# Optimization experiments

Hardware: AMD Instinct MI355X
Metric: run time of the kernel (lower is better)

Reference implementation:

```python
import jax, jax.numpy as jnp
import numpy as np

FP8_MAX = 448.0  # float8_e4m3fn max representable value


def _fp8_quant(v):
    """Snap values to the fp8 e4m3 grid (saturating), return fp32."""
    v = jnp.clip(v, -FP8_MAX, FP8_MAX)
    return v.astype(jnp.float8_e4m3fn).astype(jnp.float32)


def setup_inputs() -> dict:
    key = jax.random.key(0)
    k1, k2, k3 = jax.random.split(key, 3)
    N_TOK, D_IN, D_OUT = 8192, 4096, 4096
    x = jax.random.normal(k1, (N_TOK, D_IN), dtype=jnp.float32)
    # weight is stored already quantized to fp8 in the real module; snap to grid
    w = jax.random.normal(k2, (D_OUT, D_IN), dtype=jnp.float32)
    weight_scale = jnp.array([2.0 / FP8_MAX], dtype=jnp.float32)  # per-tensor
    weight = _fp8_quant(w / weight_scale)  # fp8-grid values, kept in fp32
    bias = jax.random.normal(k3, (D_OUT,), dtype=jnp.float32)
    input_scale = jnp.array([4.0 / FP8_MAX], dtype=jnp.float32)  # per-tensor act scale
    return {"x": x, "weight": weight, "weight_scale": weight_scale,
            "bias": bias, "input_scale": input_scale}


def reference(x, weight, weight_scale, bias, input_scale):
    # quantize_activation_per_tensor_fp8: x/scale -> clamp -> fp8 e4m3
    qinput = _fp8_quant(x / input_scale)  # [N, D_in], fp8-grid values
    acc = jnp.einsum('nk,ok->no', qinput, weight)  # fp32 accumulate
    out = acc * (input_scale * weight_scale) + bias
    return out.astype(x.dtype)
```

## Files before the change

kernel.cpp:

```cpp
#include <hip/hip_runtime.h>
#include <stdint.h>

#define FP8_MAX 448.0f

typedef float floatx16 __attribute__((ext_vector_type(16)));
typedef int   intx4    __attribute__((ext_vector_type(4)));
typedef int   intx8    __attribute__((ext_vector_type(8)));

__device__ __forceinline__ void async_copy16(const void* g, void* s) {
    __builtin_amdgcn_global_load_lds(
        (const __attribute__((address_space(1))) void*)g,
        (__attribute__((address_space(3))) void*)s,
        16, 0, 0);
}

__global__ void __launch_bounds__(256) quant_fp8_kernel(
    const float* __restrict__ x, const float* __restrict__ w,
    const float* __restrict__ scale,
    uint8_t* __restrict__ qx, uint8_t* __restrict__ qw,
    long nx4, long ntot4)
{
    const float invx = 1.0f / scale[0];
    const long stride = (long)gridDim.x * 256;
    for (long g = (long)blockIdx.x * 256 + threadIdx.x; g < ntot4; g += stride) {
        const float4* src; int* dst; float inv; long idx;
        if (g < nx4) { src = (const float4*)x; dst = (int*)qx; inv = invx; idx = g; }
        else         { src = (const float4*)w; dst = (int*)qw; inv = 1.0f; idx = g - nx4; }
        float4 v = src[idx];
        float a = fminf(fmaxf(v.x * inv, -FP8_MAX), FP8_MAX);
        float b = fminf(fmaxf(v.y * inv, -FP8_MAX), FP8_MAX);
        float c = fminf(fmaxf(v.z * inv, -FP8_MAX), FP8_MAX);
        float d = fminf(fmaxf(v.w * inv, -FP8_MAX), FP8_MAX);
        int pk = 0;
        pk = __builtin_amdgcn_cvt_pk_fp8_f32(a, b, pk, false);
        pk = __builtin_amdgcn_cvt_pk_fp8_f32(c, d, pk, true);
        dst[idx] = pk;
    }
}

__global__ void __launch_bounds__(256, 2) gemm_fp8_kernel(
    const uint8_t* __restrict__ A, const uint8_t* __restrict__ B,
    const float* __restrict__ bias,
    const float* __restrict__ in_scale, const float* __restrict__ w_scale,
    float* __restrict__ C, int M, int N, int K)
{
    __shared__ __align__(16) uint8_t As[2 * 128 * 64];
    __shared__ __align__(16) uint8_t Bs[2 * 128 * 64];

    const int tid  = threadIdx.x;
    const int lane = tid & 63;
    const int wid  = tid >> 6;
    const int wm   = wid >> 1;
    const int wn   = wid & 1;
    const int m0   = blockIdx.y * 128;
    const int n0   = blockIdx.x * 128;

    const int rl = lane & 31;
    const int h  = lane >> 5;

    const int S0 = tid, S1 = tid + 256;
    const int rA0 = S0 >> 2, cA0 = ((S0 & 3) ^ ((S0 >> 3) & 3)) * 16;
    const int rA1 = S1 >> 2, cA1 = ((S1 & 3) ^ ((S1 >> 3) & 3)) * 16;

    const uint8_t* Ab = A + (size_t)m0 * K;
    const uint8_t* Bb = B + (size_t)n0 * K;

    floatx16 acc[2][2];
#pragma unroll
    for (int i = 0; i < 2; ++i)
#pragma unroll
        for (int j = 0; j < 2; ++j)
#pragma unroll
            for (int r = 0; r < 16; ++r) acc[i][j][r] = 0.f;

    const int fsw  = (rl >> 1) & 3;
    const int ca   = ((h * 2)     ^ fsw) * 16;
    const int cb   = ((h * 2 + 1) ^ fsw) * 16;
    const int aoff = (wm * 64 + rl) * 64;
    const int boff = (wn * 64 + rl) * 64;

    const int sOne = 0x7F7F7F7F;
    const int NS = K >> 6;

    async_copy16(Ab + (size_t)rA0 * K + cA0, As + S0 * 16);
    async_copy16(Ab + (size_t)rA1 * K + cA1, As + S1 * 16);
    async_copy16(Bb + (size_t)rA0 * K + cA0, Bs + S0 * 16);
    async_copy16(Bb + (size_t)rA1 * K + cA1, Bs + S1 * 16);
    __syncthreads();

    int cur = 0;
    for (int t = 0; t < NS; ++t) {
        if (t + 1 < NS) {
            const int kt = (t + 1) << 6;
            const int nb = (cur ^ 1) * 8192;
            async_copy16(Ab + (size_t)rA0 * K + kt + cA0, As + nb + S0 * 16);
            async_copy16(Ab + (size_t)rA1 * K + kt + cA1, As + nb + S1 * 16);
            async_copy16(Bb + (size_t)rA0 * K + kt + cA0, Bs + nb + S0 * 16);
            async_copy16(Bb + (size_t)rA1 * K + kt + cA1, Bs + nb + S1 * 16);
        }

        const uint8_t* as = As + cur * 8192;
        const uint8_t* bs = Bs + cur * 8192;
        intx8 av[2], bv[2];
#pragma unroll
        for (int mi = 0; mi < 2; ++mi) {
            intx4 lo = *(const intx4*)(as + aoff + mi * 2048 + ca);
            intx4 hi = *(const intx4*)(as + aoff + mi * 2048 + cb);
            av[mi] = (intx8){lo[0], lo[1], lo[2], lo[3],
                             hi[0], hi[1], hi[2], hi[3]};
        }
#pragma unroll
        for (int ni = 0; ni < 2; ++ni) {
            intx4 lo = *(const intx4*)(bs + boff + ni * 2048 + ca);
            intx4 hi = *(const intx4*)(bs + boff + ni * 2048 + cb);
            bv[ni] = (intx8){lo[0], lo[1], lo[2], lo[3],
                             hi[0], hi[1], hi[2], hi[3]};
        }

#pragma unroll
        for (int mi = 0; mi < 2; ++mi)
#pragma unroll
            for (int ni = 0; ni < 2; ++ni)
                acc[mi][ni] = __builtin_amdgcn_mfma_scale_f32_32x32x64_f8f6f4(
                    av[mi], bv[ni], acc[mi][ni],
                    0 , 0 ,
                    0, sOne, 0, sOne);

        __syncthreads();
        cur ^= 1;
    }

    const float osc = in_scale[0] * w_scale[0];

#pragma unroll
    for (int mi = 0; mi < 2; ++mi) {
#pragma unroll
        for (int ni = 0; ni < 2; ++ni) {
            const int gn = n0 + wn * 64 + ni * 32 + rl;
            const float bvv = bias[gn];
#pragma unroll
            for (int r = 0; r < 16; ++r) {
                const int row = (r & 3) + 8 * (r >> 2) + 4 * h;
                const int gm = m0 + wm * 64 + mi * 32 + row;
                C[(size_t)gm * N + gn] = acc[mi][ni][r] * osc + bvv;
            }
        }
    }
}

extern "C" void kernel_launch(void* const* d_in, const int* in_sizes, int n_in,
                              void* d_out, int out_size, void* d_ws, size_t ws_size,
                              hipStream_t stream) {
    const float* x        = (const float*)d_in[0];
    const float* weight   = (const float*)d_in[1];
    const float* w_scale  = (const float*)d_in[2];
    const float* bias     = (const float*)d_in[3];
    const float* in_scale = (const float*)d_in[4];
    float* out = (float*)d_out;

    const int N = in_sizes[3];
    const int K = in_sizes[1] / N;
    const int M = in_sizes[0] / K;

    uint8_t* qx = (uint8_t*)d_ws;
    uint8_t* qw = (uint8_t*)d_ws + (size_t)M * K;

    const long nx4   = (long)M * K / 4;
    const long ntot4 = nx4 + (long)N * K / 4;
    long blks = (ntot4 + 255) / 256; if (blks > 2048) blks = 2048;
    quant_fp8_kernel<<<(int)blks, 256, 0, stream>>>(x, weight, in_scale,
                                                    qx, qw, nx4, ntot4);

    dim3 grid(N / 128, M / 128);
    gemm_fp8_kernel<<<grid, 256, 0, stream>>>(qx, qw, bias, in_scale, w_scale,
                                              out, M, N, K);
}
```

Measured before the change: 414.8 us.

## Enlarge GEMM tile to 256x256 with 512 threads and triple-buffered LDS pipeline

The block tile grows from 128x128 to 256x256 and the block from 256 to 512 threads. Each wave now computes a 128x64 sub-tile, which raises operand reuse from LDS and cuts global traffic per output. The double buffer becomes a three-stage LDS ring with explicit vmcnt waits, so loads run two tiles ahead, and s_setprio is raised around the MFMA block. The trade-offs are higher register pressure (8 accumulators of 16 floats), 96KB of LDS that may limit occupancy, and fewer blocks in the grid (512) to fill the CUs.

```diff
diff --git a/kernel.cpp b/kernel.cpp
--- a/kernel.cpp
+++ b/kernel.cpp
@@ -6,6 +6,9 @@
 typedef float floatx16 __attribute__((ext_vector_type(16)));
 typedef int   intx4    __attribute__((ext_vector_type(4)));
 typedef int   intx8    __attribute__((ext_vector_type(8)));
+
+#define WAIT_VMCNT_4() asm volatile("s_waitcnt vmcnt(4)" ::: "memory")
+#define WAIT_VMCNT_0() asm volatile("s_waitcnt vmcnt(0)" ::: "memory")
 
 __device__ __forceinline__ void async_copy16(const void* g, void* s) {
     __builtin_amdgcn_global_load_lds(
@@ -38,36 +41,36 @@
     }
 }
 
-__global__ void __launch_bounds__(256, 2) gemm_fp8_kernel(
+__global__ void __launch_bounds__(512, 2) gemm_fp8_kernel(
     const uint8_t* __restrict__ A, const uint8_t* __restrict__ B,
     const float* __restrict__ bias,
     const float* __restrict__ in_scale, const float* __restrict__ w_scale,
     float* __restrict__ C, int M, int N, int K)
 {
-    __shared__ __align__(16) uint8_t As[2 * 128 * 64];
-    __shared__ __align__(16) uint8_t Bs[2 * 128 * 64];
+    __shared__ __align__(16) uint8_t As[3][256 * 64];
+    __shared__ __align__(16) uint8_t Bs[3][256 * 64];
 
     const int tid  = threadIdx.x;
     const int lane = tid & 63;
     const int wid  = tid >> 6;
-    const int wm   = wid >> 1;
-    const int wn   = wid & 1;
-    const int m0   = blockIdx.y * 128;
-    const int n0   = blockIdx.x * 128;
+    const int wm   = wid >> 2;
+    const int wn   = wid & 3;
+    const int m0   = blockIdx.y * 256;
+    const int n0   = blockIdx.x * 256;
 
     const int rl = lane & 31;
     const int h  = lane >> 5;
 
-    const int S0 = tid, S1 = tid + 256;
+    const int S0 = tid, S1 = tid + 512;
     const int rA0 = S0 >> 2, cA0 = ((S0 & 3) ^ ((S0 >> 3) & 3)) * 16;
     const int rA1 = S1 >> 2, cA1 = ((S1 & 3) ^ ((S1 >> 3) & 3)) * 16;
 
     const uint8_t* Ab = A + (size_t)m0 * K;
     const uint8_t* Bb = B + (size_t)n0 * K;
 
-    floatx16 acc[2][2];
+    floatx16 acc[4][2];
 #pragma unroll
-    for (int i = 0; i < 2; ++i)
+    for (int i = 0; i < 4; ++i)
 #pragma unroll
         for (int j = 0; j < 2; ++j)
 #pragma unroll
@@ -76,39 +79,39 @@
     const int fsw  = (rl >> 1) & 3;
     const int ca   = ((h * 2)     ^ fsw) * 16;
     const int cb   = ((h * 2 + 1) ^ fsw) * 16;
-    const int aoff = (wm * 64 + rl) * 64;
-    const int boff = (wn * 64 + rl) * 64;
+    const int aoff = wm * 8192 + rl * 64;
+    const int boff = wn * 4096 + rl * 64;
 
     const int sOne = 0x7F7F7F7F;
     const int NS = K >> 6;
 
-    async_copy16(Ab + (size_t)rA0 * K + cA0, As + S0 * 16);
-    async_copy16(Ab + (size_t)rA1 * K + cA1, As + S1 * 16);
-    async_copy16(Bb + (size_t)rA0 * K + cA0, Bs + S0 * 16);
-    async_copy16(Bb + (size_t)rA1 * K + cA1, Bs + S1 * 16);
-    __syncthreads();
+    auto stage = [&](int tile, int buf) {
+        const int kt = tile << 6;
+        async_copy16(Ab + (size_t)rA0 * K + kt + cA0, As[buf] + S0 * 16);
+        async_copy16(Ab + (size_t)rA1 * K + kt + cA1, As[buf] + S1 * 16);
+        async_copy16(Bb + (size_t)rA0 * K + kt + cA0, Bs[buf] + S0 * 16);
+        async_copy16(Bb + (size_t)rA1 * K + kt + cA1, Bs[buf] + S1 * 16);
+    };
 
-    int cur = 0;
+    stage(0, 0);
+    stage(1, 1);
+
+    int cur = 0, stg = 2;
     for (int t = 0; t < NS; ++t) {
-        if (t + 1 < NS) {
-            const int kt = (t + 1) << 6;
-            const int nb = (cur ^ 1) * 8192;
-            async_copy16(Ab + (size_t)rA0 * K + kt + cA0, As + nb + S0 * 16);
-            async_copy16(Ab + (size_t)rA1 * K + kt + cA1, As + nb + S1 * 16);
-            async_copy16(Bb + (size_t)rA0 * K + kt + cA0, Bs + nb + S0 * 16);
-            async_copy16(Bb + (size_t)rA1 * K + kt + cA1, Bs + nb + S1 * 16);
+        if (t < NS - 1) { WAIT_VMCNT_4(); }
+        else            { WAIT_VMCNT_0(); }
+        __builtin_amdgcn_s_barrier();
+        __builtin_amdgcn_sched_barrier(0);
+
+        if (t + 2 < NS) {
+            stage(t + 2, stg);
+            stg = (stg == 2) ? 0 : stg + 1;
         }
 
-        const uint8_t* as = As + cur * 8192;
-        const uint8_t* bs = Bs + cur * 8192;
-        intx8 av[2], bv[2];
-#pragma unroll
-        for (int mi = 0; mi < 2; ++mi) {
-            intx4 lo = *(const intx4*)(as + aoff + mi * 2048 + ca);
-            intx4 hi = *(const intx4*)(as + aoff + mi * 2048 + cb);
-            av[mi] = (intx8){lo[0], lo[1], lo[2], lo[3],
-                             hi[0], hi[1], hi[2], hi[3]};
-        }
+        const uint8_t* as = As[cur];
+        const uint8_t* bs = Bs[cur];
+
+        intx8 bv[2];
 #pragma unroll
         for (int ni = 0; ni < 2; ++ni) {
             intx4 lo = *(const intx4*)(bs + boff + ni * 2048 + ca);
@@ -117,23 +120,27 @@
                              hi[0], hi[1], hi[2], hi[3]};
         }
 
+        __builtin_amdgcn_s_setprio(1);
 #pragma unroll
-        for (int mi = 0; mi < 2; ++mi)
-#pragma unroll
-            for (int ni = 0; ni < 2; ++ni)
-                acc[mi][ni] = __builtin_amdgcn_mfma_scale_f32_32x32x64_f8f6f4(
-                    av[mi], bv[ni], acc[mi][ni],
-                    0 , 0 ,
-                    0, sOne, 0, sOne);
+        for (int mi = 0; mi < 4; ++mi) {
+            intx4 lo = *(const intx4*)(as + aoff + mi * 2048 + ca);
+            intx4 hi = *(const intx4*)(as + aoff + mi * 2048 + cb);
+            intx8 av = (intx8){lo[0], lo[1], lo[2], lo[3],
+                               hi[0], hi[1], hi[2], hi[3]};
+            acc[mi][0] = __builtin_amdgcn_mfma_scale_f32_32x32x64_f8f6f4(
+                av, bv[0], acc[mi][0], 0, 0, 0, sOne, 0, sOne);
+            acc[mi][1] = __builtin_amdgcn_mfma_scale_f32_32x32x64_f8f6f4(
+                av, bv[1], acc[mi][1], 0, 0, 0, sOne, 0, sOne);
+        }
+        __builtin_amdgcn_s_setprio(0);
 
-        __syncthreads();
-        cur ^= 1;
+        cur = (cur == 2) ? 0 : cur + 1;
     }
 
     const float osc = in_scale[0] * w_scale[0];
 
 #pragma unroll
-    for (int mi = 0; mi < 2; ++mi) {
+    for (int mi = 0; mi < 4; ++mi) {
 #pragma unroll
         for (int ni = 0; ni < 2; ++ni) {
             const int gn = n0 + wn * 64 + ni * 32 + rl;
@@ -141,7 +148,7 @@
 #pragma unroll
             for (int r = 0; r < 16; ++r) {
                 const int row = (r & 3) + 8 * (r >> 2) + 4 * h;
-                const int gm = m0 + wm * 64 + mi * 32 + row;
+                const int gm = m0 + wm * 128 + mi * 32 + row;
                 C[(size_t)gm * N + gn] = acc[mi][ni][r] * osc + bvv;
             }
         }
@@ -171,7 +178,7 @@
     quant_fp8_kernel<<<(int)blks, 256, 0, stream>>>(x, weight, in_scale,
                                                     qx, qw, nx4, ntot4);
 
-    dim3 grid(N / 128, M / 128);
-    gemm_fp8_kernel<<<grid, 256, 0, stream>>>(qx, qw, bias, in_scale, w_scale,
+    dim3 grid(N / 256, M / 256);
+    gemm_fp8_kernel<<<grid, 512, 0, stream>>>(qx, qw, bias, in_scale, w_scale,
                                               out, M, N, K);
 }
```

After: 431.0 us. +3.9%, slower.
